# Optimization experiments

Hardware: AMD Instinct MI355X
Metric: run time of the kernel (lower is better)

## Reference

```python
import jax, jax.numpy as jnp
import numpy as np

L, D, F, V = 24, 1024, 4096, 50277  # n_layer, n_embd, ffn hidden (4*D), vocab
RESCALE = 6


def _ln(x, w, b, eps=1e-5):
    m = jnp.mean(x, axis=-1, keepdims=True)
    v = jnp.mean(jnp.square(x - m), axis=-1, keepdims=True)
    return (x - m) * jax.lax.rsqrt(v + eps) * w + b


def setup_inputs() -> dict:
    key = jax.random.key(0)
    ks = iter(jax.random.split(key, 64))

    def nrm(shape, s=0.02):
        return jax.random.normal(next(ks), shape, jnp.float32) * s

    def uni(shape):
        return jax.random.uniform(next(ks), shape, jnp.float32)

    state = jnp.zeros((L, 5, D), jnp.float32).at[:, 4, :].set(-1e30)  # pp init
    return {
        "token_embd": jax.random.normal(next(ks), (D,), jnp.float32),
        "state": state,
        "emb_ln_w": jnp.ones((D,), jnp.float32),
        "emb_ln_b": jnp.zeros((D,), jnp.float32),
        "ln1_w": jnp.ones((L, D), jnp.float32),
        "ln1_b": jnp.zeros((L, D), jnp.float32),
        "ln2_w": jnp.ones((L, D), jnp.float32),
        "ln2_b": jnp.zeros((L, D), jnp.float32),
        "att_tmk": uni((L, D)),
        "att_tmv": uni((L, D)),
        "att_tmr": uni((L, D)),
        "att_tf": nrm((L, D), 0.5),
        "att_td": -jnp.exp(nrm((L, D), 0.5)),  # time_decay = -exp(w) at load
        "att_kw": nrm((L, D, D)),
        "att_vw": nrm((L, D, D)),
        "att_rw": nrm((L, D, D)),
        "att_ow": nrm((L, D, D)),
        "ffn_tmk": uni((L, D)),
        "ffn_tmr": uni((L, D)),
        "ffn_kw": nrm((L, F, D)),
        "ffn_vw": nrm((L, D, F)),
        "ffn_rw": nrm((L, D, D)),
        "out_ln_w": jnp.ones((D,), jnp.float32),
        "out_ln_b": jnp.zeros((D,), jnp.float32),
        "head_w": nrm((V, D)),
    }


def reference(token_embd, state, emb_ln_w, emb_ln_b, ln1_w, ln1_b, ln2_w, ln2_b,
              att_tmk, att_tmv, att_tmr, att_tf, att_td, att_kw, att_vw, att_rw,
              att_ow, ffn_tmk, ffn_tmr, ffn_kw, ffn_vw, ffn_rw,
              out_ln_w, out_ln_b, head_w):
    x0 = _ln(token_embd, emb_ln_w, emb_ln_b)  # encoder

    def layer(x, inputs):
        (i, st, l1w, l1b, l2w, l2b, tmk, tmv, tmr, tf, td,
         kw, vw, rw, ow, ftmk, ftmr, fkw, fvw, frw) = inputs
        # ---- time mixing ----
        xn = _ln(x, l1w, l1b)
        s_att, aa, bb, pp = st[1], st[2], st[3], st[4]
        xk = xn * tmk + s_att * (1 - tmk)
        xv = xn * tmv + s_att * (1 - tmv)
        xr = xn * tmr + s_att * (1 - tmr)
        r = jax.nn.sigmoid(rw @ xr)
        kk = kw @ xk
        vv = vw @ xv
        ww = tf + kk
        p = jnp.maximum(pp, ww)
        e1 = jnp.exp(pp - p)
        e2 = jnp.exp(ww - p)
        a = e1 * aa + e2 * vv
        b = e1 * bb + e2
        ww2 = pp + td
        p2 = jnp.maximum(ww2, kk)
        f1 = jnp.exp(ww2 - p2)
        f2 = jnp.exp(kk - p2)
        new_aa = f1 * aa + f2 * vv
        new_bb = f1 * bb + f2
        x = x + ow @ (r * (a / b))
        # ---- channel mixing ----
        xn2 = _ln(x, l2w, l2b)
        s_ffn = st[0]
        xk2 = xn2 * ftmk + s_ffn * (1 - ftmk)
        xr2 = xn2 * ftmr + s_ffn * (1 - ftmr)
        r2 = jax.nn.sigmoid(frw @ xr2)
        k2 = jnp.square(jax.nn.relu(fkw @ xk2))
        x = x + r2 * (fvw @ k2)
        # rescale every RESCALE layers
        x = jnp.where((i + 1) % RESCALE == 0, x * 0.5, x)
        new_st = jnp.stack([xn2, xn, new_aa, new_bb, p2])
        return x, new_st

    idx = jnp.arange(L)
    x, new_state = jax.lax.scan(
        layer, x0,
        (idx, state, ln1_w, ln1_b, ln2_w, ln2_b, att_tmk, att_tmv, att_tmr,
         att_tf, att_td, att_kw, att_vw, att_rw, att_ow, ffn_tmk, ffn_tmr,
         ffn_kw, ffn_vw, ffn_rw))
    logits = head_w @ _ln(x, out_ln_w, out_ln_b)  # decoder
    return logits, new_state
```

## Files before the change

### kernel.cpp

```cpp
#include <hip/hip_runtime.h>

#define DD 1024
#define FF 4096
#define LL 24
#define VV 50277
#define NB 1024
#define AG __HIP_MEMORY_SCOPE_AGENT

typedef unsigned u32;
typedef float v4f __attribute__((ext_vector_type(4)));


__device__ __forceinline__ float wave_sum(float v) {
#pragma unroll
    for (int o = 32; o > 0; o >>= 1) v += __shfl_xor(v, o, 64);
    return v;
}

__device__ __forceinline__ v4f ln_fast(v4f x, const float* __restrict__ w,
                                       const float* __restrict__ b,
                                       float* scr, int t) {
    float s1 = x[0] + x[1] + x[2] + x[3];
    float s2 = x[0]*x[0] + x[1]*x[1] + x[2]*x[2] + x[3]*x[3];
    s1 = wave_sum(s1); s2 = wave_sum(s2);
    int wv = t >> 6;
    __syncthreads();
    if ((t & 63) == 0) { scr[wv] = s1; scr[4 + wv] = s2; }
    __syncthreads();
    float S1 = scr[0] + scr[1] + scr[2] + scr[3];
    float S2 = scr[4] + scr[5] + scr[6] + scr[7];
    float m = S1 * (1.0f / 1024.0f);
    float var = S2 * (1.0f / 1024.0f) - m * m;
    float rs = rsqrtf(var + 1e-5f);
    v4f w4 = ((const v4f*)w)[t], b4 = ((const v4f*)b)[t];
    return (x - m) * rs * w4 + b4;
}

__device__ __forceinline__ v4f mixv(v4f n, v4f s, v4f m) { return n * m + s * (1.0f - m); }

__device__ __forceinline__ float dotv(v4f a, v4f x) {
    return fmaf(a[0], x[0], fmaf(a[1], x[1], fmaf(a[2], x[2], a[3] * x[3])));
}

struct Row { v4f a, b, c, d; };

__device__ __forceinline__ void row_load(Row& r, const float* p, int lane) {
    const v4f* q = (const v4f*)p;
    r.a = q[lane]; r.b = q[lane + 64]; r.c = q[lane + 128]; r.d = q[lane + 192];
}
__device__ __forceinline__ void row_pin(Row& r) {
    asm volatile("" : "+v"(r.a), "+v"(r.b), "+v"(r.c), "+v"(r.d));
}
__device__ __forceinline__ float row_dot(const Row& r, const v4f* v, int lane) {
    return dotv(r.a, v[lane]) + dotv(r.b, v[lane + 64]) +
           dotv(r.c, v[lane + 128]) + dotv(r.d, v[lane + 192]);
}


__device__ __forceinline__ void astore_f(float* p, float v) {
    __hip_atomic_store(p, v, __ATOMIC_RELAXED, AG);
}
__device__ __forceinline__ void cload(v4f& d, const float* p) {
    asm volatile("global_load_dwordx4 %0, %1, off sc0 sc1" : "=v"(d) : "v"(p));
}
__device__ __forceinline__ void cwait1(v4f& a) {
    asm volatile("s_waitcnt vmcnt(0)" : "+v"(a));
}
__device__ __forceinline__ void cwait4(v4f& a, v4f& b, v4f& c, v4f& d) {
    asm volatile("s_waitcnt vmcnt(0)" : "+v"(a), "+v"(b), "+v"(c), "+v"(d));
}


__device__ __forceinline__ void gbar(u32* sync, u32 ev, int b, int t) {
    __syncthreads();
    if (t == 0) {
        u32* shard = sync + (b & 7) * 32;
        u32* l2c   = sync + 8 * 32;
        u32* rel0  = sync + 9 * 32;
        u32 old = __hip_atomic_fetch_add(shard, 1u, __ATOMIC_RELAXED, AG);
        if (old == 128u * ev - 1u) {
            u32 o2 = __hip_atomic_fetch_add(l2c, 1u, __ATOMIC_RELAXED, AG);
            if (o2 == 8u * ev - 1u) {
#pragma unroll
                for (int i = 0; i < 8; ++i)
                    __hip_atomic_store(rel0 + i * 32, ev, __ATOMIC_RELAXED, AG);
            }
        }
        u32* myrel = rel0 + (b & 7) * 32;
        while (__hip_atomic_load(myrel, __ATOMIC_RELAXED, AG) < ev)
            __builtin_amdgcn_s_sleep(2);
    }
    __syncthreads();
}


__global__ __launch_bounds__(256, 4) void rwkv_all(
    const float* __restrict__ token_embd, const float* __restrict__ state,
    const float* __restrict__ emb_ln_w, const float* __restrict__ emb_ln_b,
    const float* __restrict__ ln1_w, const float* __restrict__ ln1_b,
    const float* __restrict__ ln2_w, const float* __restrict__ ln2_b,
    const float* __restrict__ att_tmk, const float* __restrict__ att_tmv,
    const float* __restrict__ att_tmr, const float* __restrict__ att_tf,
    const float* __restrict__ att_td,
    const float* __restrict__ att_kw, const float* __restrict__ att_vw,
    const float* __restrict__ att_rw, const float* __restrict__ att_ow,
    const float* __restrict__ ffn_tmk, const float* __restrict__ ffn_tmr,
    const float* __restrict__ ffn_kw, const float* __restrict__ ffn_vw,
    const float* __restrict__ ffn_rw,
    const float* __restrict__ out_ln_w, const float* __restrict__ out_ln_b,
    const float* __restrict__ head_w,
    float* __restrict__ logits, float* __restrict__ st_out_base,
    float* __restrict__ ws, u32* __restrict__ sync) {

    __shared__ __align__(16) v4f s_buf[1024];
    __shared__ __align__(16) v4f s_vec[256];
    __shared__ float scr[8];
    __shared__ float s_kvr[3];
    __shared__ float s_part[8];
    __shared__ float s_xsave;

    const int t = threadIdx.x, lane = t & 63, w = t >> 6, b = blockIdx.x;

    float* rab = ws;
    float* xB  = ws + 1024;
    float* k2  = ws + 2048;
    float* xD  = ws + 6144;

    v4f xv = ((const v4f*)token_embd)[t];
    xv = ln_fast(xv, emb_ln_w, emb_ln_b, scr, t);

    u32 ev = 0;
#pragma unroll 1
    for (int i = 0; i < LL; ++i) {
        const size_t oD = (size_t)i * DD;
        const float* st = state + (size_t)i * 5 * DD;
        float* sto = st_out_base + (size_t)i * 5 * DD;
        const float scale = ((i + 1) % 6 == 0) ? 0.5f : 1.0f;

        if (i > 0) { cload(xv, xD + 4 * t); cwait1(xv); }
        if (t == (b >> 2)) s_xsave = xv[b & 3];
        v4f n = ln_fast(xv, ln1_w + oD, ln1_b + oD, scr, t);
        if (b == 0) ((v4f*)(sto + DD))[t] = n;
        {
            v4f sa = ((const v4f*)(st + DD))[t];
            s_buf[t]       = mixv(n, sa, ((const v4f*)(att_tmk + oD))[t]);
            s_buf[256 + t] = mixv(n, sa, ((const v4f*)(att_tmv + oD))[t]);
            s_buf[512 + t] = mixv(n, sa, ((const v4f*)(att_tmr + oD))[t]);
        }
        Row rB;
        if (w == 3) { row_load(rB, att_ow + oD * DD + (size_t)b * DD, lane); row_pin(rB); }
        __syncthreads();
        if (w < 3) {
            Row R;
            row_load(R, (w == 0 ? att_kw : w == 1 ? att_vw : att_rw)
                        + oD * DD + (size_t)b * DD, lane);
            float acc = wave_sum(row_dot(R, &s_buf[w * 256], lane));
            if (lane == 0) s_kvr[w] = acc;
        }
        __syncthreads();
        if (t == 0) {
            float kk = s_kvr[0], vv = s_kvr[1];
            float rr = 1.0f / (1.0f + expf(-s_kvr[2]));
            float aa = st[2 * DD + b], bb = st[3 * DD + b], pp = st[4 * DD + b];
            float ww = att_tf[oD + b] + kk;
            float p = fmaxf(pp, ww);
            float e1 = expf(pp - p), e2 = expf(ww - p);
            astore_f(rab + b, rr * ((e1 * aa + e2 * vv) / (e1 * bb + e2)));
            float ww2 = pp + att_td[oD + b];
            float p2 = fmaxf(ww2, kk);
            float f1 = expf(ww2 - p2), f2 = expf(kk - p2);
            sto[2 * DD + b] = f1 * aa + f2 * vv;
            sto[3 * DD + b] = f1 * bb + f2;
            sto[4 * DD + b] = p2;
        }
        gbar(sync, ++ev, b, t);

        { v4f rv; cload(rv, rab + 4 * t); cwait1(rv); s_vec[t] = rv; }
        __syncthreads();
        if (w == 3) {
            float acc = wave_sum(row_dot(rB, &s_vec[0], lane));
            if (lane == 0) astore_f(xB + b, s_xsave + acc);
        }
        gbar(sync, ++ev, b, t);

        cload(xv, xB + 4 * t); cwait1(xv);
        if (t == (b >> 2)) s_xsave = xv[b & 3];
        n = ln_fast(xv, ln2_w + oD, ln2_b + oD, scr, t);
        if (b == 0) ((v4f*)sto)[t] = n;
        {
            v4f sf = ((const v4f*)st)[t];
            s_buf[t]       = mixv(n, sf, ((const v4f*)(ffn_tmk + oD))[t]);
            s_buf[256 + t] = mixv(n, sf, ((const v4f*)(ffn_tmr + oD))[t]);
        }
        __syncthreads();
        {
            Row R;
            row_load(R, ffn_kw + (size_t)i * FF * DD + (size_t)(4 * b + w) * DD, lane);
            float acc = wave_sum(row_dot(R, &s_buf[0], lane));
            if (lane == 0) { float rl = fmaxf(acc, 0.f); astore_f(k2 + 4 * b + w, rl * rl); }
            v4f fq = ((const v4f*)(ffn_rw + (size_t)i * DD * DD + (size_t)b * DD))[w * 64 + lane];
            float pr = wave_sum(dotv(fq, s_buf[256 + w * 64 + lane]));
            if (lane == 0) s_part[w] = pr;
        }
        gbar(sync, ++ev, b, t);

        {
            v4f q0, q1, q2, q3;
            cload(q0, k2 + 4 * t);        cload(q1, k2 + 4 * t + 1024);
            cload(q2, k2 + 4 * t + 2048); cload(q3, k2 + 4 * t + 3072);
            cwait4(q0, q1, q2, q3);
            s_buf[t] = q0; s_buf[256 + t] = q1; s_buf[512 + t] = q2; s_buf[768 + t] = q3;
        }
        __syncthreads();
        {
            const v4f* W4 = (const v4f*)(ffn_vw + (size_t)i * DD * FF + (size_t)b * FF)
                            + (size_t)w * 256;
            float acc = 0.f;
#pragma unroll
            for (int k = 0; k < 4; ++k)
                acc += dotv(W4[lane + 64 * k], s_buf[w * 256 + lane + 64 * k]);
            acc = wave_sum(acc);
            if (lane == 0) s_part[4 + w] = acc;
        }
        __syncthreads();
        if (t == 0) {
            float r2v = 1.0f / (1.0f + expf(-(s_part[0] + s_part[1] + s_part[2] + s_part[3])));
            float dsum = s_part[4] + s_part[5] + s_part[6] + s_part[7];
            astore_f(xD + b, (s_xsave + r2v * dsum) * scale);
        }
        gbar(sync, ++ev, b, t);
    }

    cload(xv, xD + 4 * t); cwait1(xv);
    v4f nh = ln_fast(xv, out_ln_w, out_ln_b, scr, t);
    s_vec[t] = nh;
    __syncthreads();
#pragma unroll 1
    for (int j = 0; j < 13; ++j) {
        int row = j * 4096 + 4 * b + w;
        if (row < VV) {
            Row rh;
            row_load(rh, head_w + (size_t)row * DD, lane);
            float acc = wave_sum(row_dot(rh, &s_vec[0], lane));
            if (lane == 0) logits[row] = acc;
        }
    }
}


extern "C" void kernel_launch(void* const* d_in, const int* in_sizes, int n_in,
                              void* d_out, int out_size, void* d_ws, size_t ws_size,
                              hipStream_t stream) {
    const float* token_embd = (const float*)d_in[0];
    const float* state      = (const float*)d_in[1];
    const float* emb_ln_w   = (const float*)d_in[2];
    const float* emb_ln_b   = (const float*)d_in[3];
    const float* ln1_w      = (const float*)d_in[4];
    const float* ln1_b      = (const float*)d_in[5];
    const float* ln2_w      = (const float*)d_in[6];
    const float* ln2_b      = (const float*)d_in[7];
    const float* att_tmk    = (const float*)d_in[8];
    const float* att_tmv    = (const float*)d_in[9];
    const float* att_tmr    = (const float*)d_in[10];
    const float* att_tf     = (const float*)d_in[11];
    const float* att_td     = (const float*)d_in[12];
    const float* att_kw     = (const float*)d_in[13];
    const float* att_vw     = (const float*)d_in[14];
    const float* att_rw     = (const float*)d_in[15];
    const float* att_ow     = (const float*)d_in[16];
    const float* ffn_tmk    = (const float*)d_in[17];
    const float* ffn_tmr    = (const float*)d_in[18];
    const float* ffn_kw     = (const float*)d_in[19];
    const float* ffn_vw     = (const float*)d_in[20];
    const float* ffn_rw     = (const float*)d_in[21];
    const float* out_ln_w   = (const float*)d_in[22];
    const float* out_ln_b   = (const float*)d_in[23];
    const float* head_w     = (const float*)d_in[24];

    float* logits = (float*)d_out;
    float* st_out_base = (float*)d_out + VV;

    float* ws = (float*)d_ws;
    u32* sync = (u32*)(ws + 8192);

    hipMemsetAsync(sync, 0, 4096, stream);

    rwkv_all<<<NB, 256, 0, stream>>>(
        token_embd, state, emb_ln_w, emb_ln_b, ln1_w, ln1_b, ln2_w, ln2_b,
        att_tmk, att_tmv, att_tmr, att_tf, att_td,
        att_kw, att_vw, att_rw, att_ow,
        ffn_tmk, ffn_tmr, ffn_kw, ffn_vw, ffn_rw,
        out_ln_w, out_ln_b, head_w,
        logits, st_out_base, ws, sync);
}
```

Before: 664.1 us.

## Prefetch next-stage weight rows into registers before each grid barrier

Each weight row that a phase needs (attention k/v/r/o, ffn key, ffn receptance, ffn value) is now loaded into registers before the preceding grid barrier, and the next layer's attention rows are loaded at the end of the current layer. This hides global-memory latency for the weight streams behind the barrier waits instead of exposing it after each barrier. In exchange, register pressure rises from several live Row buffers, which could lower occupancy or cause spills.

```diff
diff --git a/kernel.cpp b/kernel.cpp
--- a/kernel.cpp
+++ b/kernel.cpp
@@ -126,6 +126,11 @@
     float* k2  = ws + 2048;
     float* xD  = ws + 6144;
 
+    Row rA;
+    row_load(rA, (w == 0 ? att_kw : w == 1 ? att_vw : w == 2 ? att_rw : att_ow)
+                 + (size_t)b * DD, lane);
+    row_pin(rA);
+
     v4f xv = ((const v4f*)token_embd)[t];
     xv = ln_fast(xv, emb_ln_w, emb_ln_b, scr, t);
 
@@ -147,14 +152,9 @@
             s_buf[256 + t] = mixv(n, sa, ((const v4f*)(att_tmv + oD))[t]);
             s_buf[512 + t] = mixv(n, sa, ((const v4f*)(att_tmr + oD))[t]);
         }
-        Row rB;
-        if (w == 3) { row_load(rB, att_ow + oD * DD + (size_t)b * DD, lane); row_pin(rB); }
         __syncthreads();
         if (w < 3) {
-            Row R;
-            row_load(R, (w == 0 ? att_kw : w == 1 ? att_vw : att_rw)
-                        + oD * DD + (size_t)b * DD, lane);
-            float acc = wave_sum(row_dot(R, &s_buf[w * 256], lane));
+            float acc = wave_sum(row_dot(rA, &s_buf[w * 256], lane));
             if (lane == 0) s_kvr[w] = acc;
         }
         __syncthreads();
@@ -173,14 +173,19 @@
             sto[3 * DD + b] = f1 * bb + f2;
             sto[4 * DD + b] = p2;
         }
+        Row rFK;
+        row_load(rFK, ffn_kw + (size_t)i * FF * DD + (size_t)(4 * b + w) * DD, lane);
+        row_pin(rFK);
         gbar(sync, ++ev, b, t);
 
         { v4f rv; cload(rv, rab + 4 * t); cwait1(rv); s_vec[t] = rv; }
         __syncthreads();
         if (w == 3) {
-            float acc = wave_sum(row_dot(rB, &s_vec[0], lane));
+            float acc = wave_sum(row_dot(rA, &s_vec[0], lane));
             if (lane == 0) astore_f(xB + b, s_xsave + acc);
         }
+        v4f frq = ((const v4f*)(ffn_rw + (size_t)i * DD * DD + (size_t)b * DD))[w * 64 + lane];
+        asm volatile("" : "+v"(frq));
         gbar(sync, ++ev, b, t);
 
         cload(xv, xB + 4 * t); cwait1(xv);
@@ -194,14 +199,14 @@
         }
         __syncthreads();
         {
-            Row R;
-            row_load(R, ffn_kw + (size_t)i * FF * DD + (size_t)(4 * b + w) * DD, lane);
-            float acc = wave_sum(row_dot(R, &s_buf[0], lane));
+            float acc = wave_sum(row_dot(rFK, &s_buf[0], lane));
             if (lane == 0) { float rl = fmaxf(acc, 0.f); astore_f(k2 + 4 * b + w, rl * rl); }
-            v4f fq = ((const v4f*)(ffn_rw + (size_t)i * DD * DD + (size_t)b * DD))[w * 64 + lane];
-            float pr = wave_sum(dotv(fq, s_buf[256 + w * 64 + lane]));
+            float pr = wave_sum(dotv(frq, s_buf[256 + w * 64 + lane]));
             if (lane == 0) s_part[w] = pr;
         }
+        Row rFV;
+        row_load(rFV, ffn_vw + (size_t)i * DD * FF + (size_t)b * FF + (size_t)w * 1024, lane);
+        row_pin(rFV);
         gbar(sync, ++ev, b, t);
 
         {
@@ -213,12 +218,11 @@
         }
         __syncthreads();
         {
-            const v4f* W4 = (const v4f*)(ffn_vw + (size_t)i * DD * FF + (size_t)b * FF)
-                            + (size_t)w * 256;
             float acc = 0.f;
-#pragma unroll
-            for (int k = 0; k < 4; ++k)
-                acc += dotv(W4[lane + 64 * k], s_buf[w * 256 + lane + 64 * k]);
+            acc += dotv(rFV.a, s_buf[w * 256 + lane]);
+            acc += dotv(rFV.b, s_buf[w * 256 + lane + 64]);
+            acc += dotv(rFV.c, s_buf[w * 256 + lane + 128]);
+            acc += dotv(rFV.d, s_buf[w * 256 + lane + 192]);
             acc = wave_sum(acc);
             if (lane == 0) s_part[4 + w] = acc;
         }
@@ -227,6 +231,11 @@
             float r2v = 1.0f / (1.0f + expf(-(s_part[0] + s_part[1] + s_part[2] + s_part[3])));
             float dsum = s_part[4] + s_part[5] + s_part[6] + s_part[7];
             astore_f(xD + b, (s_xsave + r2v * dsum) * scale);
+        }
+        if (i + 1 < LL) {
+            row_load(rA, (w == 0 ? att_kw : w == 1 ? att_vw : w == 2 ? att_rw : att_ow)
+                         + (size_t)(i + 1) * DD * DD + (size_t)b * DD, lane);
+            row_pin(rA);
         }
         gbar(sync, ++ev, b, t);
     }
```

Measured after the change: 695.4 us. 1.05x slower.
